# Kernel tuning notes

Measured on AMD Instinct MI355X. Metric: run time of the kernel, lower is better.

## Reference

```python
import jax, jax.numpy as jnp
import numpy as np
import math

NUM_STEPS = 100
SIGMA_R, SIGMA_T = 0.05, 0.03
B, HO = 4096, 64

def _alpha_bars(n=NUM_STEPS):
    # squaredcos_cap_v2 schedule (betas_for_alpha_bar), then cumprod of alphas via log-cumsum-exp
    def ab(t):
        return math.cos((t + 0.008) / 1.008 * math.pi / 2) ** 2
    betas = np.array([min(1.0 - ab((i + 1) / n) / ab(i / n), 0.999) for i in range(n)], np.float64)
    return np.exp(np.cumsum(np.log(1.0 - betas))).astype(np.float32)

def _hat(w):
    x, y, z = w[..., 0], w[..., 1], w[..., 2]
    o = jnp.zeros_like(x)
    return jnp.stack([
        jnp.stack([o, -z, y], -1),
        jnp.stack([z, o, -x], -1),
        jnp.stack([-y, x, o], -1)], -2)

def se3_exp(xi):
    # xi: (...,6) = [omega(3), v(3)]  (rotation first, matching sigma_r/sigma_t ordering)
    w, v = xi[..., :3], xi[..., 3:]
    th2 = jnp.sum(w * w, -1)
    small = th2 < 1e-8
    th2s = jnp.where(small, 1.0, th2)
    th = jnp.sqrt(th2s)
    A = jnp.where(small, 1.0 - th2 / 6.0, jnp.sin(th) / th)
    Bc = jnp.where(small, 0.5 - th2 / 24.0, (1.0 - jnp.cos(th)) / th2s)
    Cc = jnp.where(small, 1.0 / 6.0 - th2 / 120.0, (th - jnp.sin(th)) / (th2s * th))
    K = _hat(w)
    K2 = K @ K
    I3 = jnp.eye(3, dtype=xi.dtype)
    R = I3 + A[..., None, None] * K + Bc[..., None, None] * K2
    V = I3 + Bc[..., None, None] * K + Cc[..., None, None] * K2
    t = jnp.einsum('...ij,...j->...i', V, v)
    top = jnp.concatenate([R, t[..., None]], -1)  # (...,3,4)
    bot = jnp.broadcast_to(jnp.array([0., 0., 0., 1.], xi.dtype), top.shape[:-2] + (1, 4))
    return jnp.concatenate([top, bot], -2)

def se3_log(H):
    # H: (...,4,4) -> (...,6) = [omega, v]
    R = H[..., :3, :3]
    t = H[..., :3, 3]
    vee = 0.5 * jnp.stack([R[..., 2, 1] - R[..., 1, 2],
                           R[..., 0, 2] - R[..., 2, 0],
                           R[..., 1, 0] - R[..., 0, 1]], -1)  # sin(theta)*axis
    cos_t = jnp.clip(0.5 * (jnp.trace(R, axis1=-2, axis2=-1) - 1.0), -1.0, 1.0)
    s2 = jnp.sum(vee * vee, -1)  # sin(theta)^2
    small = s2 < 1e-12
    sin_s = jnp.sqrt(jnp.where(small, 1.0, s2))
    th = jnp.arctan2(sin_s, cos_t)  # valid in the non-small branch
    fac = jnp.where(small, 1.0 + s2 / 6.0, th / sin_s)  # theta / sin(theta)
    w = fac[..., None] * vee
    # V^{-1} = I - K/2 + D * K^2 ; D -> 1/12 as theta -> 0
    one_m_cos = jnp.where(small, 1.0, 1.0 - cos_t)
    th2s = jnp.where(small, 1.0, th * th)
    D = jnp.where(small, 1.0 / 12.0 + s2 / 720.0,
                  (1.0 - th * sin_s / (2.0 * one_m_cos)) / th2s)
    K = _hat(w)
    I3 = jnp.eye(3, dtype=H.dtype)
    Vinv = I3 - 0.5 * K + D[..., None, None] * (K @ K)
    v = jnp.einsum('...ij,...j->...i', Vinv, t)
    return jnp.concatenate([w, v], -1)

def _add_noise(twist, noise, alpha_bars, timesteps):
    original = se3_exp(twist)                 # (B,Ho,4,4) valid SE(3) samples
    ab = alpha_bars[timesteps][:, None, None]  # (B,1,1)
    H_inv = jnp.linalg.inv(original)           # H_T @ inv(orig) with H_T = I
    xi = se3_log(H_inv)
    H_t = se3_exp((1.0 - jnp.sqrt(ab)) * xi) @ original
    scale = jnp.concatenate([jnp.full((3,), SIGMA_R, jnp.float32),
                             jnp.full((3,), SIGMA_T, jnp.float32)])
    n = jnp.sqrt(1.0 - ab) * scale * noise
    H_noise = se3_exp(n)
    return H_noise @ H_t, H_noise

def setup_inputs() -> dict:
    key = jax.random.key(0)
    k1, k2, k3 = jax.random.split(key, 3)
    twist = 0.5 * jax.random.normal(k1, (B, HO, 6), jnp.float32)  # keeps angle << pi
    noise = jax.random.normal(k2, (B, HO, 6), jnp.float32)
    timesteps = jax.random.randint(k3, (B,), 0, NUM_STEPS)
    return {"twist": twist, "noise": noise,
            "alpha_bars": jnp.asarray(_alpha_bars()), "timesteps": timesteps}

def reference(twist, noise, alpha_bars, timesteps):
    return _add_noise(twist, noise, alpha_bars, timesteps)
```

## Files before the change

kernel.cpp:

```cpp
#include <hip/hip_runtime.h>
#include <math.h>

constexpr int B_DIM = 4096;
constexpr int HO_DIM = 64;
constexpr int NTOT = B_DIM * HO_DIM;
constexpr int QTOT = NTOT * 4;
constexpr int NBLK = QTOT / 256;
constexpr float SIGMA_R = 0.05f;
constexpr float SIGMA_T = 0.03f;

typedef float f4 __attribute__((ext_vector_type(4)));
typedef float f2 __attribute__((ext_vector_type(2)));

__device__ __forceinline__ void exp_se3(float x, float y, float z,
                                        float vx, float vy, float vz,
                                        float R[9], float t[3]) {
    float th2 = x*x + y*y + z*z;
    bool small = th2 < 1e-8f;
    float th2s = small ? 1.0f : th2;
    float th = __builtin_amdgcn_sqrtf(th2s);
    float s = __sinf(th);
    float c = __cosf(th);
    float rth  = __builtin_amdgcn_rcpf(th);
    float rth2 = rth * rth;
    float A  = small ? (1.0f - th2 * (1.0f/6.0f))        : (s * rth);
    float Bc = small ? (0.5f - th2 * (1.0f/24.0f))       : ((1.0f - c) * rth2);
    float Cc = small ? (1.0f/6.0f - th2 * (1.0f/120.0f)) : ((th - s) * rth2 * rth);
    R[0] = 1.0f + Bc*(x*x - th2);
    R[1] = -A*z + Bc*x*y;
    R[2] =  A*y + Bc*x*z;
    R[3] =  A*z + Bc*x*y;
    R[4] = 1.0f + Bc*(y*y - th2);
    R[5] = -A*x + Bc*y*z;
    R[6] = -A*y + Bc*x*z;
    R[7] =  A*x + Bc*y*z;
    R[8] = 1.0f + Bc*(z*z - th2);
    float V0 = 1.0f + Cc*(x*x - th2);
    float V1 = -Bc*z + Cc*x*y;
    float V2 =  Bc*y + Cc*x*z;
    float V3 =  Bc*z + Cc*x*y;
    float V4 = 1.0f + Cc*(y*y - th2);
    float V5 = -Bc*x + Cc*y*z;
    float V6 = -Bc*y + Cc*x*z;
    float V7 =  Bc*x + Cc*y*z;
    float V8 = 1.0f + Cc*(z*z - th2);
    t[0] = V0*vx + V1*vy + V2*vz;
    t[1] = V3*vx + V4*vy + V5*vz;
    t[2] = V6*vx + V7*vy + V8*vz;
}

__global__ __launch_bounds__(256) void DiffusionScheduler_kernel(
    const float* __restrict__ twist, const float* __restrict__ noise,
    const float* __restrict__ alpha_bars, const int* __restrict__ timesteps,
    float* __restrict__ out)
{
    int k = blockIdx.x * 256 + threadIdx.x;
    int mat = k >> 2;
    int rr  = k & 3;

    int ts = timesteps[blockIdx.x];
    float ab = alpha_bars[ts];
    float sab = __builtin_amdgcn_sqrtf(ab);
    float sq  = __builtin_amdgcn_sqrtf(1.0f - ab);
    float kr = sq * SIGMA_R, kt = sq * SIGMA_T;

    const f2* nz = (const f2*)(noise + 6 * (size_t)mat);
    f2 n0 = nz[0], n1 = nz[1], n2 = nz[2];
    const f2* tw = (const f2*)(twist + 6 * (size_t)mat);
    f2 a0 = tw[0], a1 = tw[1], a2 = tw[2];

    float Rn[9], tn[3];
    exp_se3(kr*n0.x, kr*n0.y, kr*n1.x, kt*n1.y, kt*n2.x, kt*n2.y, Rn, tn);

    float Rt[9], tt[3];
    exp_se3(sab*a0.x, sab*a0.y, sab*a1.x, sab*a1.y, sab*a2.x, sab*a2.y, Rt, tt);

    float q0 = rr==0 ? Rn[0] : (rr==1 ? Rn[3] : Rn[6]);
    float q1 = rr==0 ? Rn[1] : (rr==1 ? Rn[4] : Rn[7]);
    float q2 = rr==0 ? Rn[2] : (rr==1 ? Rn[5] : Rn[8]);
    float qt = rr==0 ? tn[0] : (rr==1 ? tn[1] : tn[2]);

    float r0 = q0*Rt[0] + q1*Rt[3] + q2*Rt[6];
    float r1 = q0*Rt[1] + q1*Rt[4] + q2*Rt[7];
    float r2 = q0*Rt[2] + q1*Rt[5] + q2*Rt[8];
    float r3 = q0*tt[0] + q1*tt[1] + q2*tt[2] + qt;

    f4 row0 = (rr == 3) ? (f4){0.0f, 0.0f, 0.0f, 1.0f} : (f4){r0, r1, r2, r3};
    f4 row1 = (rr == 3) ? (f4){0.0f, 0.0f, 0.0f, 1.0f} : (f4){q0, q1, q2, qt};

    ((f4*)out)[k] = row0;
    ((f4*)(out + (size_t)NTOT * 16))[k] = row1;
}

extern "C" void kernel_launch(void* const* d_in, const int* in_sizes, int n_in,
                              void* d_out, int out_size, void* d_ws, size_t ws_size,
                              hipStream_t stream) {
    const float* twist       = (const float*)d_in[0];
    const float* noise       = (const float*)d_in[1];
    const float* alpha_bars  = (const float*)d_in[2];
    const int*   timesteps   = (const int*)d_in[3];
    float* out = (float*)d_out;

    dim3 block(256);
    dim3 grid(NBLK);
    hipLaunchKernelGGL(DiffusionScheduler_kernel, grid, block, 0, stream,
                       twist, noise, alpha_bars, timesteps, out);
}
```

Baseline: 15.02 us.

## Compute one matrix per thread and stage outputs through LDS for coalesced stores

Each thread now handles one whole pose instead of one output row. Before, four threads each recomputed both SE(3) exponentials for the same pose. Outputs are transposed through shared memory so the float4 global stores stay contiguous. This removes the fourfold redundant transcendental math but adds LDS traffic, a block barrier, and about 33KB of shared memory per block, which may lower occupancy.

```diff
diff --git a/kernel.cpp b/kernel.cpp
--- a/kernel.cpp
+++ b/kernel.cpp
@@ -4,8 +4,8 @@
 constexpr int B_DIM = 4096;
 constexpr int HO_DIM = 64;
 constexpr int NTOT = B_DIM * HO_DIM;
-constexpr int QTOT = NTOT * 4;
-constexpr int NBLK = QTOT / 256;
+constexpr int MPB  = 256;
+constexpr int NBLK = NTOT / MPB;
 constexpr float SIGMA_R = 0.05f;
 constexpr float SIGMA_T = 0.03f;
 
@@ -54,19 +54,21 @@
     const float* __restrict__ alpha_bars, const int* __restrict__ timesteps,
     float* __restrict__ out)
 {
-    int k = blockIdx.x * 256 + threadIdx.x;
-    int mat = k >> 2;
-    int rr  = k & 3;
+    __shared__ float lds0[16][258];
+    __shared__ float lds1[16][258];
 
-    int ts = timesteps[blockIdx.x];
+    int t = threadIdx.x;
+    size_t mat = (size_t)blockIdx.x * MPB + t;
+
+    int ts = timesteps[mat >> 6];
     float ab = alpha_bars[ts];
     float sab = __builtin_amdgcn_sqrtf(ab);
     float sq  = __builtin_amdgcn_sqrtf(1.0f - ab);
     float kr = sq * SIGMA_R, kt = sq * SIGMA_T;
 
-    const f2* nz = (const f2*)(noise + 6 * (size_t)mat);
+    const f2* nz = (const f2*)(noise + 6 * mat);
     f2 n0 = nz[0], n1 = nz[1], n2 = nz[2];
-    const f2* tw = (const f2*)(twist + 6 * (size_t)mat);
+    const f2* tw = (const f2*)(twist + 6 * mat);
     f2 a0 = tw[0], a1 = tw[1], a2 = tw[2];
 
     float Rn[9], tn[3];
@@ -75,21 +77,47 @@
     float Rt[9], tt[3];
     exp_se3(sab*a0.x, sab*a0.y, sab*a1.x, sab*a1.y, sab*a2.x, sab*a2.y, Rt, tt);
 
-    float q0 = rr==0 ? Rn[0] : (rr==1 ? Rn[3] : Rn[6]);
-    float q1 = rr==0 ? Rn[1] : (rr==1 ? Rn[4] : Rn[7]);
-    float q2 = rr==0 ? Rn[2] : (rr==1 ? Rn[5] : Rn[8]);
-    float qt = rr==0 ? tn[0] : (rr==1 ? tn[1] : tn[2]);
+    float R0[9], t0[3];
+    #pragma unroll
+    for (int r = 0; r < 3; ++r) {
+        #pragma unroll
+        for (int cdx = 0; cdx < 3; ++cdx) {
+            R0[3*r+cdx] = Rn[3*r+0]*Rt[0+cdx] + Rn[3*r+1]*Rt[3+cdx] + Rn[3*r+2]*Rt[6+cdx];
+        }
+    }
+    t0[0] = Rn[0]*tt[0]+Rn[1]*tt[1]+Rn[2]*tt[2] + tn[0];
+    t0[1] = Rn[3]*tt[0]+Rn[4]*tt[1]+Rn[5]*tt[2] + tn[1];
+    t0[2] = Rn[6]*tt[0]+Rn[7]*tt[1]+Rn[8]*tt[2] + tn[2];
 
-    float r0 = q0*Rt[0] + q1*Rt[3] + q2*Rt[6];
-    float r1 = q0*Rt[1] + q1*Rt[4] + q2*Rt[7];
-    float r2 = q0*Rt[2] + q1*Rt[5] + q2*Rt[8];
-    float r3 = q0*tt[0] + q1*tt[1] + q2*tt[2] + qt;
+    lds0[ 0][t] = R0[0]; lds0[ 1][t] = R0[1]; lds0[ 2][t] = R0[2]; lds0[ 3][t] = t0[0];
+    lds0[ 4][t] = R0[3]; lds0[ 5][t] = R0[4]; lds0[ 6][t] = R0[5]; lds0[ 7][t] = t0[1];
+    lds0[ 8][t] = R0[6]; lds0[ 9][t] = R0[7]; lds0[10][t] = R0[8]; lds0[11][t] = t0[2];
+    lds0[12][t] = 0.0f;  lds0[13][t] = 0.0f;  lds0[14][t] = 0.0f;  lds0[15][t] = 1.0f;
 
-    f4 row0 = (rr == 3) ? (f4){0.0f, 0.0f, 0.0f, 1.0f} : (f4){r0, r1, r2, r3};
-    f4 row1 = (rr == 3) ? (f4){0.0f, 0.0f, 0.0f, 1.0f} : (f4){q0, q1, q2, qt};
+    lds1[ 0][t] = Rn[0]; lds1[ 1][t] = Rn[1]; lds1[ 2][t] = Rn[2]; lds1[ 3][t] = tn[0];
+    lds1[ 4][t] = Rn[3]; lds1[ 5][t] = Rn[4]; lds1[ 6][t] = Rn[5]; lds1[ 7][t] = tn[1];
+    lds1[ 8][t] = Rn[6]; lds1[ 9][t] = Rn[7]; lds1[10][t] = Rn[8]; lds1[11][t] = tn[2];
+    lds1[12][t] = 0.0f;  lds1[13][t] = 0.0f;  lds1[14][t] = 0.0f;  lds1[15][t] = 1.0f;
 
-    ((f4*)out)[k] = row0;
-    ((f4*)(out + (size_t)NTOT * 16))[k] = row1;
+    __syncthreads();
+
+    int rr = t & 3;
+    int mb = t >> 2;
+    f4* o0 = ((f4*)out) + (size_t)blockIdx.x * (MPB * 4);
+    f4* o1 = o0 + (size_t)NTOT * 4;
+
+    #pragma unroll
+    for (int c = 0; c < 4; ++c) {
+        int m = c * 64 + mb;
+        f4 v = {lds0[4*rr+0][m], lds0[4*rr+1][m], lds0[4*rr+2][m], lds0[4*rr+3][m]};
+        o0[c * 256 + t] = v;
+    }
+    #pragma unroll
+    for (int c = 0; c < 4; ++c) {
+        int m = c * 64 + mb;
+        f4 v = {lds1[4*rr+0][m], lds1[4*rr+1][m], lds1[4*rr+2][m], lds1[4*rr+3][m]};
+        o1[c * 256 + t] = v;
+    }
 }
 
 extern "C" void kernel_launch(void* const* d_in, const int* in_sizes, int n_in,
```

Result: faster. 13.81 us (-8.0%).
